# Optimization experiments

Measured on AMD Instinct MI355X. Metric: run time of the kernel, lower is better.

## Reference

```python
import jax, jax.numpy as jnp
import numpy as np

B, D, H = 64, 2048, 2048


def setup_inputs() -> dict:
    key = jax.random.key(0)
    ks = jax.random.split(key, 10)
    s = 1.0 / np.sqrt(D)  # Linear init scale
    # small z scale keeps exp() gates in a sane range
    return {
        "t": jnp.zeros((), jnp.float32),
        "z": jax.random.normal(ks[0], (B, D), jnp.float32) * 0.02,
        "K": jax.random.normal(ks[1], (B, D), jnp.float32) * 0.02,
        "V": jax.random.normal(ks[2], (B, D, D), jnp.float32) * 0.02,
        "Wq": jax.random.normal(ks[3], (D, D), jnp.float32) * s,
        "bq": jnp.zeros((D,), jnp.float32),
        "Wk": jax.random.normal(ks[4], (D, D), jnp.float32) * s,
        "bk": jnp.zeros((D,), jnp.float32),
        "Wv": jax.random.normal(ks[5], (D, D), jnp.float32) * s,
        "bv": jnp.zeros((D,), jnp.float32),
        "W1": jax.random.normal(ks[6], (D, H), jnp.float32) * s,
        "b1": jnp.zeros((H,), jnp.float32),
        "W2": jax.random.normal(ks[7], (H, D), jnp.float32) * (1.0 / np.sqrt(H)),
        "b2": jnp.zeros((D,), jnp.float32),
    }


def reference(t, z, K, V, Wq, bq, Wk, bk, Wv, bv, W1, b1, W2, b2):
    # get_ode_gradient_nn: 2-layer tanh MLP (stand-in for user ode_func_net)
    dz = jnp.tanh(z @ W1 + b1) @ W2 + b2                 # [B, D]
    dK = jnp.exp(z @ Wk + bk)                            # exp gate, [B, D]
    v = z @ Wv + bv                                      # [B, D]
    dV = jnp.einsum("bd,be->bde", v, dK)                # rank-1 outer update, [B, D, D]
    q = jnp.exp(z @ Wq + bq)                             # [B, D]
    a = jnp.sum(q * dK, axis=-1, keepdims=True)          # q . dK, [B, 1]
    dq = q * (dz @ Wq + bq)                              # [B, D]
    da = a + jnp.sum(dq * K, axis=-1, keepdims=True)     # [B, 1]
    dc = jnp.einsum("bde,be->bd", dV, q) + jnp.einsum("bde,be->bd", V, dq)  # [B, D]
    return (dz, da, dc, dK, dV)
```

## Files before the change

### kernel.cpp

```cpp
#include <hip/hip_runtime.h>
#include <cstddef>
#include <math.h>

#define BB 64
#define DD 2048
#define HH 2048
#define BD (BB*DD)
#define WN (2048*2048)

typedef unsigned short u16;
typedef __attribute__((ext_vector_type(8))) short bf16x8;
typedef __attribute__((ext_vector_type(4))) float f32x4;
typedef __attribute__((ext_vector_type(4))) float f4;

__device__ __forceinline__ u16 f2b(float x) {
    union { float f; unsigned u; } v; v.f = x;
    unsigned r = v.u + 0x7FFFu + ((v.u >> 16) & 1u);
    return (u16)(r >> 16);
}

__device__ __forceinline__ void gload16(const void* g, void* l) {
    __builtin_amdgcn_global_load_lds(
        (__attribute__((address_space(1))) void*)g,
        (__attribute__((address_space(3))) void*)l, 16, 0, 0);
}


__global__ __launch_bounds__(256) void wconv(
    const float* __restrict__ W0, const float* __restrict__ W1,
    const float* __restrict__ W2, const float* __restrict__ W3,
    const float* __restrict__ W4, u16* __restrict__ wt)
{
    const float* W;
    switch (blockIdx.z) {
        case 0: W = W0; break; case 1: W = W1; break;
        case 2: W = W2; break; case 3: W = W3; break;
        default: W = W4; break;
    }
    u16* T = wt + (size_t)blockIdx.z * WN;

    __shared__ u16 tile[64][66];
    int k0 = blockIdx.x * 64, n0 = blockIdx.y * 64;
    int t = threadIdx.x;
    {
        int r = t >> 2, c0 = (t & 3) * 16;
        const float* src = W + (size_t)(k0 + r) * DD + n0 + c0;
#pragma unroll
        for (int q = 0; q < 4; ++q) {
            float4 f = *(const float4*)(src + q * 4);
            tile[r][c0 + q*4 + 0] = f2b(f.x);
            tile[r][c0 + q*4 + 1] = f2b(f.y);
            tile[r][c0 + q*4 + 2] = f2b(f.z);
            tile[r][c0 + q*4 + 3] = f2b(f.w);
        }
    }
    __syncthreads();
    {
        int rn = t >> 2, ck = (t & 3) * 16;
        u16 o[16];
#pragma unroll
        for (int j = 0; j < 16; ++j) o[j] = tile[ck + j][rn];
        u16* dst = T + (size_t)(n0 + rn) * DD + k0 + ck;
        *(bf16x8*)dst       = *(bf16x8*)&o[0];
        *(bf16x8*)(dst + 8) = *(bf16x8*)&o[8];
    }
}

__global__ __launch_bounds__(256) void zconv(
    const float* __restrict__ z, u16* __restrict__ zb)
{
    int i = (blockIdx.x * 256 + threadIdx.x) * 4;
    float4 f = *(const float4*)&z[i];
    union { u16 u[4]; uint2 v; } o;
    o.u[0] = f2b(f.x); o.u[1] = f2b(f.y); o.u[2] = f2b(f.z); o.u[3] = f2b(f.w);
    *(uint2*)&zb[i] = o.v;
}

__device__ __forceinline__ void gemm_bf16_body(
    const u16* __restrict__ A, const u16* __restrict__ Wt,
    float* __restrict__ P, int kc)
{
    __shared__ u16 Als[64 * 32];
    __shared__ u16 Wls[64 * 32];
    const int t = threadIdx.x, w = t >> 6, lane = t & 63;
    const int n0 = blockIdx.x * 64;
    const int k0 = blockIdx.y * kc;

    f32x4 acc[4];
#pragma unroll
    for (int mt = 0; mt < 4; ++mt) acc[mt] = (f32x4){0.f, 0.f, 0.f, 0.f};

    const int srow = lane >> 2;
    const int sk   = (lane & 3) * 8;
    const u16* gA = A  + (size_t)(w * 16 + srow) * DD + k0 + sk;
    const u16* gW = Wt + (size_t)(n0 + w * 16 + srow) * DD + k0 + sk;
    u16* lA = &Als[w * 512];
    u16* lW = &Wls[w * 512];

    const int lane15 = lane & 15;
    const int k8 = (lane >> 4) * 8;

    for (int kk = 0; kk < kc; kk += 32) {
        gload16(gA, lA);
        gload16(gW, lW);
        gA += 32; gW += 32;
        __syncthreads();

        bf16x8 bfrag = *(const bf16x8*)&Wls[(w * 16 + lane15) * 32 + k8];
#pragma unroll
        for (int mt = 0; mt < 4; ++mt) {
            bf16x8 afrag = *(const bf16x8*)&Als[(mt * 16 + lane15) * 32 + k8];
            acc[mt] = __builtin_amdgcn_mfma_f32_16x16x32_bf16(
                afrag, bfrag, acc[mt], 0, 0, 0);
        }
        __syncthreads();
    }

    const int col = n0 + w * 16 + lane15;
    const int r4 = (lane >> 4) * 4;
#pragma unroll
    for (int mt = 0; mt < 4; ++mt)
#pragma unroll
        for (int j = 0; j < 4; ++j)
            P[(size_t)(mt * 16 + r4 + j) * DD + col] = acc[mt][j];
}

__global__ __launch_bounds__(256) void gemm_bf16_single(
    const u16* __restrict__ A, const u16* __restrict__ Wt,
    float* __restrict__ part, int kc)
{
    float* P = part + (size_t)blockIdx.y * 64 * DD;
    gemm_bf16_body(A, Wt, P, kc);
}

__global__ __launch_bounds__(256) void gemm_bf16_kv(
    const u16* __restrict__ A, const u16* __restrict__ Wkt,
    const u16* __restrict__ Wvt, float* __restrict__ p0,
    float* __restrict__ p1, int kc)
{
    const u16* Wt = blockIdx.z ? Wvt : Wkt;
    float* P = (blockIdx.z ? p1 : p0) + (size_t)blockIdx.y * 64 * DD;
    gemm_bf16_body(A, Wt, P, kc);
}

__global__ __launch_bounds__(256) void gemm_bf16_q(
    const u16* __restrict__ zb, const u16* __restrict__ dzb,
    const u16* __restrict__ Wqt, float* __restrict__ part, int kc)
{
    const u16* A = blockIdx.z ? dzb : zb;
    float* P = part + ((size_t)blockIdx.y * 128 + blockIdx.z * 64) * DD;
    gemm_bf16_body(A, Wqt, P, kc);
}

__global__ __launch_bounds__(256) void ep_h(
    const float* __restrict__ p, const float* __restrict__ b1,
    u16* __restrict__ hb, int KS)
{
    int i = blockIdx.x * 256 + threadIdx.x;
    float s = b1[i & (DD - 1)];
    for (int ks = 0; ks < KS; ++ks) s += p[(size_t)ks * BD + i];
    hb[i] = f2b(tanhf(s));
}

__global__ __launch_bounds__(256) void ep_dz(
    const float* __restrict__ p, const float* __restrict__ b2,
    float* __restrict__ dz, u16* __restrict__ dzb, int KS)
{
    int i = blockIdx.x * 256 + threadIdx.x;
    float s = b2[i & (DD - 1)];
    for (int ks = 0; ks < KS; ++ks) s += p[(size_t)ks * BD + i];
    dz[i]  = s;
    dzb[i] = f2b(s);
}

__global__ __launch_bounds__(256) void ep_kv(
    const float* __restrict__ pk, const float* __restrict__ pv,
    const float* __restrict__ bk, const float* __restrict__ bv,
    float* __restrict__ dKo, float* __restrict__ vo, int KS)
{
    int i = blockIdx.x * 256 + threadIdx.x;
    int d = i & (DD - 1);
    float sk = 0.f, sv = 0.f;
    for (int ks = 0; ks < KS; ++ks) {
        sk += pk[(size_t)ks * BD + i];
        sv += pv[(size_t)ks * BD + i];
    }
    dKo[i] = expf(sk + bk[d]);
    vo[i]  = sv + bv[d];
}

__global__ __launch_bounds__(256) void ep_q_dq(
    const float* __restrict__ pq, const float* __restrict__ bq,
    float* __restrict__ qo, float* __restrict__ dqo, int KS)
{
    int i = blockIdx.x * 256 + threadIdx.x;
    int b = i >> 11, d = i & (DD - 1);
    float sq = 0.f, sd = 0.f;
    for (int ks = 0; ks < KS; ++ks) {
        const float* P = pq + (size_t)ks * (128 * DD);
        sq += P[(size_t)b * DD + d];
        sd += P[(size_t)(b + 64) * DD + d];
    }
    float bb = bq[d];
    float qv = expf(sq + bb);
    qo[i]  = qv;
    dqo[i] = qv * (sd + bb);
}

template<int MT>
__device__ __forceinline__ void gemm_body_f32(
    const float* __restrict__ A0, const float* __restrict__ A1,
    const float* __restrict__ W, float* __restrict__ part, int kc)
{
    constexpr int KC = 32;
    constexpr int RT = MT / 16;
    __shared__ float As[KC][MT];
    __shared__ float Ws[KC][64];

    const int t  = threadIdx.x;
    const int n0 = blockIdx.x * 64;
    const int k0 = blockIdx.y * kc;
    const int i  = t >> 4;
    const int j  = t & 15;

    float acc[RT][4];
#pragma unroll
    for (int r = 0; r < RT; ++r)
#pragma unroll
        for (int c = 0; c < 4; ++c) acc[r][c] = 0.f;

    for (int kk0 = 0; kk0 < kc; kk0 += KC) {
        {
            int kk = t >> 3;
            int nn = (t & 7) << 3;
            const float* s = W + (size_t)(k0 + kk0 + kk) * DD + n0 + nn;
            *(float4*)&Ws[kk][nn]     = *(const float4*)s;
            *(float4*)&Ws[kk][nn + 4] = *(const float4*)(s + 4);
        }
        if constexpr (MT == 64) {
            int m  = t & 63;
            int kb = (t >> 6) << 3;
            const float* s = A0 + (size_t)m * DD + k0 + kk0 + kb;
            float4 a0 = *(const float4*)s;
            float4 a1 = *(const float4*)(s + 4);
            As[kb+0][m] = a0.x; As[kb+1][m] = a0.y;
            As[kb+2][m] = a0.z; As[kb+3][m] = a0.w;
            As[kb+4][m] = a1.x; As[kb+5][m] = a1.y;
            As[kb+6][m] = a1.z; As[kb+7][m] = a1.w;
        } else {
            int m  = t & 127;
            int kb = (t >> 7) << 4;
            const float* base = (m < 64) ? (A0 + (size_t)m * DD)
                                         : (A1 + (size_t)(m - 64) * DD);
            const float* s = base + k0 + kk0 + kb;
#pragma unroll
            for (int p = 0; p < 4; ++p) {
                float4 av = *(const float4*)(s + p * 4);
                As[kb+p*4+0][m] = av.x; As[kb+p*4+1][m] = av.y;
                As[kb+p*4+2][m] = av.z; As[kb+p*4+3][m] = av.w;
            }
        }
        __syncthreads();
#pragma unroll
        for (int kk = 0; kk < KC; ++kk) {
            float4 wv = *(float4*)&Ws[kk][j << 2];
#pragma unroll
            for (int rq = 0; rq < RT / 4; ++rq) {
                float4 av = *(float4*)&As[kk][i * RT + rq * 4];
                acc[rq*4+0][0] = fmaf(av.x, wv.x, acc[rq*4+0][0]);
                acc[rq*4+0][1] = fmaf(av.x, wv.y, acc[rq*4+0][1]);
                acc[rq*4+0][2] = fmaf(av.x, wv.z, acc[rq*4+0][2]);
                acc[rq*4+0][3] = fmaf(av.x, wv.w, acc[rq*4+0][3]);
                acc[rq*4+1][0] = fmaf(av.y, wv.x, acc[rq*4+1][0]);
                acc[rq*4+1][1] = fmaf(av.y, wv.y, acc[rq*4+1][1]);
                acc[rq*4+1][2] = fmaf(av.y, wv.z, acc[rq*4+1][2]);
                acc[rq*4+1][3] = fmaf(av.y, wv.w, acc[rq*4+1][3]);
                acc[rq*4+2][0] = fmaf(av.z, wv.x, acc[rq*4+2][0]);
                acc[rq*4+2][1] = fmaf(av.z, wv.y, acc[rq*4+2][1]);
                acc[rq*4+2][2] = fmaf(av.z, wv.z, acc[rq*4+2][2]);
                acc[rq*4+2][3] = fmaf(av.z, wv.w, acc[rq*4+2][3]);
                acc[rq*4+3][0] = fmaf(av.w, wv.x, acc[rq*4+3][0]);
                acc[rq*4+3][1] = fmaf(av.w, wv.y, acc[rq*4+3][1]);
                acc[rq*4+3][2] = fmaf(av.w, wv.z, acc[rq*4+3][2]);
                acc[rq*4+3][3] = fmaf(av.w, wv.w, acc[rq*4+3][3]);
            }
        }
        __syncthreads();
    }

    float* P = part + (size_t)blockIdx.y * MT * DD + n0 + (j << 2);
#pragma unroll
    for (int r = 0; r < RT; ++r)
        *(float4*)&P[(size_t)(i * RT + r) * DD] =
            make_float4(acc[r][0], acc[r][1], acc[r][2], acc[r][3]);
}

__global__ __launch_bounds__(256) void gemm64(
    const float* __restrict__ A, const float* __restrict__ W,
    float* __restrict__ part, int kc)
{ gemm_body_f32<64>(A, A, W, part, kc); }

__global__ __launch_bounds__(256) void gemm64_z2(
    const float* __restrict__ A,
    const float* __restrict__ W0, const float* __restrict__ W1,
    float* __restrict__ p0, float* __restrict__ p1, int kc)
{
    const float* W = blockIdx.z ? W1 : W0;
    float*       P = blockIdx.z ? p1 : p0;
    gemm_body_f32<64>(A, A, W, P, kc);
}

__global__ __launch_bounds__(256) void gemm128(
    const float* __restrict__ A0, const float* __restrict__ A1,
    const float* __restrict__ W, float* __restrict__ part, int kc)
{ gemm_body_f32<128>(A0, A1, W, part, kc); }

__global__ __launch_bounds__(256) void epilogue_f32(
    const float* __restrict__ part, const float* __restrict__ bias,
    float* __restrict__ out, int act, int KS)
{
    int i = blockIdx.x * 256 + threadIdx.x;
    float s = bias[i & (DD - 1)];
    for (int ks = 0; ks < KS; ++ks) s += part[(size_t)ks * BD + i];
    if (act == 1) s = tanhf(s);
    out[i] = s;
}

__global__ __launch_bounds__(256) void reduce_a_da(
    const float* __restrict__ q, const float* __restrict__ dK,
    const float* __restrict__ dq, const float* __restrict__ Kin,
    float* __restrict__ a_ws, float* __restrict__ da_out)
{
    int b = blockIdx.x;
    int t = threadIdx.x;
    const float* qb  = q   + (size_t)b * DD;
    const float* dKb = dK  + (size_t)b * DD;
    const float* dqb = dq  + (size_t)b * DD;
    const float* Kb  = Kin + (size_t)b * DD;

    float s1 = 0.f, s2 = 0.f;
    for (int i = t; i < DD; i += 256) {
        s1 = fmaf(qb[i],  dKb[i], s1);
        s2 = fmaf(dqb[i], Kb[i],  s2);
    }
#pragma unroll
    for (int off = 32; off; off >>= 1) {
        s1 += __shfl_down(s1, off);
        s2 += __shfl_down(s2, off);
    }
    __shared__ float r1[4], r2[4];
    if ((t & 63) == 0) { r1[t >> 6] = s1; r2[t >> 6] = s2; }
    __syncthreads();
    if (t == 0) {
        float a  = r1[0] + r1[1] + r1[2] + r1[3];
        float k2 = r2[0] + r2[1] + r2[2] + r2[3];
        a_ws[b]   = a;
        da_out[b] = a + k2;
    }
}

__global__ __launch_bounds__(256) void fused_dv_dc(
    const float* __restrict__ V, const float* __restrict__ v,
    const float* __restrict__ dK, const float* __restrict__ dq,
    const float* __restrict__ a, float* __restrict__ dV,
    float* __restrict__ dc)
{
    int b     = blockIdx.x >> 5;
    int chunk = blockIdx.x & 31;
    int wave  = threadIdx.x >> 6;
    int lane  = threadIdx.x & 63;

    const f4* dK4 = (const f4*)(dK + ((size_t)b << 11));
    const f4* dq4 = (const f4*)(dq + ((size_t)b << 11));
    f4 dKr[8], dqr[8];
#pragma unroll
    for (int u = 0; u < 8; ++u) {
        dKr[u] = dK4[u * 64 + lane];
        dqr[u] = dq4[u * 64 + lane];
    }
    float ab = a[b];
    int row0 = chunk * 64 + wave * 16;

    for (int g = 0; g < 4; ++g) {
        float dot[4];
#pragma unroll
        for (int r2 = 0; r2 < 4; ++r2) {
            int row = row0 + g * 4 + r2;
            size_t off = ((size_t)((b << 11) | row)) << 11;
            const f4* V4  = (const f4*)(V  + off);
            f4*       dV4 = (f4*)(dV + off);
            float vr = v[((size_t)b << 11) + row];
            float d  = 0.f;
#pragma unroll
            for (int u = 0; u < 8; ++u) {
                f4 Vv = __builtin_nontemporal_load(&V4[u * 64 + lane]);
                d += Vv[0] * dqr[u][0] + Vv[1] * dqr[u][1]
                   + Vv[2] * dqr[u][2] + Vv[3] * dqr[u][3];
                f4 o = vr * dKr[u];
                __builtin_nontemporal_store(o, &dV4[u * 64 + lane]);
            }
            dot[r2] = d;
        }
#pragma unroll
        for (int r2 = 0; r2 < 4; ++r2) {
            float d = dot[r2];
#pragma unroll
            for (int s = 32; s; s >>= 1) d += __shfl_down(d, s);
            if (lane == 0) {
                int row = row0 + g * 4 + r2;
                dc[((size_t)b << 11) + row] =
                    v[((size_t)b << 11) + row] * ab + d;
            }
        }
    }
}

extern "C" void kernel_launch(void* const* d_in, const int* in_sizes, int n_in,
                              void* d_out, int out_size, void* d_ws, size_t ws_size,
                              hipStream_t stream)
{
    const float* z   = (const float*)d_in[1];
    const float* Kin = (const float*)d_in[2];
    const float* Vin = (const float*)d_in[3];
    const float* Wq  = (const float*)d_in[4];
    const float* bq  = (const float*)d_in[5];
    const float* Wk  = (const float*)d_in[6];
    const float* bk  = (const float*)d_in[7];
    const float* Wv  = (const float*)d_in[8];
    const float* bv  = (const float*)d_in[9];
    const float* W1  = (const float*)d_in[10];
    const float* b1  = (const float*)d_in[11];
    const float* W2  = (const float*)d_in[12];
    const float* b2  = (const float*)d_in[13];

    float* out   = (float*)d_out;
    float* o_dz  = out;
    float* o_da  = out + BD;
    float* o_dc  = out + BD + BB;
    float* o_dK  = out + 2 * BD + BB;
    float* o_dV  = out + 3 * BD + BB;

    float* ws    = (float*)d_ws;
    float* ws_v  = ws;
    float* ws_q  = ws + BD;
    float* ws_dq = ws + 2 * BD;
    float* ws_a  = ws + 3 * BD;
    float* ws_h  = ws + 3 * BD + 64;
    u16*   zb    = (u16*)(ws + 4 * BD + 64);
    u16*   hb    = zb + BD;
    u16*   dzb   = hb + BD;
    u16*   wt    = dzb + BD;
    float* poolb = (float*)(wt + 5ull * WN);

    const size_t pre_fl = 4ull * BD + 64 + (3ull * BD + 5ull * WN) / 2;

    int KS = 0;
    for (int ks = 16; ks >= 4; ks >>= 1)
        if ((pre_fl + 2ull * ks * BD) * 4ull <= ws_size) { KS = ks; break; }

    dim3 blk(256);
    dim3 gE(BD / 256);

    if (KS) {
        int kc = DD / KS;
        float* p0 = poolb;
        float* p1 = poolb + (size_t)KS * BD;

        dim3 gW(32, 32, 5);
        dim3 gG(32, KS);
        dim3 gG2(32, KS, 2);

        wconv<<<gW, blk, 0, stream>>>(W1, W2, Wk, Wv, Wq, wt);
        zconv<<<dim3(BD / 1024), blk, 0, stream>>>(z, zb);

        u16* W1t = wt;
        u16* W2t = wt + 1ull * WN;
        u16* Wkt = wt + 2ull * WN;
        u16* Wvt = wt + 3ull * WN;
        u16* Wqt = wt + 4ull * WN;

        gemm_bf16_single<<<gG, blk, 0, stream>>>(zb, W1t, p0, kc);
        ep_h<<<gE, blk, 0, stream>>>(p0, b1, hb, KS);

        gemm_bf16_single<<<gG, blk, 0, stream>>>(hb, W2t, p0, kc);
        ep_dz<<<gE, blk, 0, stream>>>(p0, b2, o_dz, dzb, KS);

        gemm_bf16_kv<<<gG2, blk, 0, stream>>>(zb, Wkt, Wvt, p0, p1, kc);
        ep_kv<<<gE, blk, 0, stream>>>(p0, p1, bk, bv, o_dK, ws_v, KS);

        gemm_bf16_q<<<gG2, blk, 0, stream>>>(zb, dzb, Wqt, p0, kc);
        ep_q_dq<<<gE, blk, 0, stream>>>(p0, bq, ws_q, ws_dq, KS);
    } else {
        float* pool = ws + 4 * BD + 64;
        int KSf = 16;
        while (KSf > 1 &&
               ((size_t)(4 * BD + 64) + 2ull * KSf * BD) * 4ull > ws_size)
            KSf >>= 1;
        int kc = DD / KSf;
        float* p0 = pool;
        float* p1 = pool + (size_t)KSf * BD;

        dim3 gG(DD / 64, KSf);
        dim3 gG2(DD / 64, KSf, 2);

        gemm64<<<gG, blk, 0, stream>>>(z, W1, p0, kc);
        epilogue_f32<<<gE, blk, 0, stream>>>(p0, b1, ws_h, 1, KSf);

        gemm64<<<gG, blk, 0, stream>>>(ws_h, W2, p0, kc);
        epilogue_f32<<<gE, blk, 0, stream>>>(p0, b2, o_dz, 0, KSf);

        gemm64_z2<<<gG2, blk, 0, stream>>>(z, Wk, Wv, p0, p1, kc);
        ep_kv<<<gE, blk, 0, stream>>>(p0, p1, bk, bv, o_dK, ws_v, KSf);

        gemm128<<<gG, blk, 0, stream>>>(z, o_dz, Wq, p0, kc);
        ep_q_dq<<<gE, blk, 0, stream>>>(p0, bq, ws_q, ws_dq, KSf);
    }

    reduce_a_da<<<dim3(BB), blk, 0, stream>>>(ws_q, o_dK, ws_dq, Kin, ws_a, o_da);

    fused_dv_dc<<<dim3(BB * 32), blk, 0, stream>>>(Vin, ws_v, o_dK, ws_dq, ws_a,
                                                   o_dV, o_dc);
}
```

Measured before the change: 493.9 us.

## Split fused dV/dc kernel and merge z conversion into weight conversion

The fused kernel that both wrote dV and read V for dc is split into two kernels. dv_write is launched right after the K/V epilogue, and dc_dot runs at the end. The zconv launch is folded into wconv as an extra z-slice of the grid, saving one launch. The split aims to avoid mixing the write and read streams in one kernel, but it adds a separate launch and keeps the same total traffic (256MB write plus 256MB read) on a serial stream, so no overlap is gained.

Measured after the change: 445.7 us. -9.8%, faster.

```diff
diff --git a/kernel.cpp b/kernel.cpp
--- a/kernel.cpp
+++ b/kernel.cpp
@@ -29,8 +29,24 @@
 __global__ __launch_bounds__(256) void wconv(
     const float* __restrict__ W0, const float* __restrict__ W1,
     const float* __restrict__ W2, const float* __restrict__ W3,
-    const float* __restrict__ W4, u16* __restrict__ wt)
-{
+    const float* __restrict__ W4, u16* __restrict__ wt,
+    const float* __restrict__ z, u16* __restrict__ zb)
+{
+    int t = threadIdx.x;
+    if (blockIdx.z == 5) {
+        if (blockIdx.y != 0 || blockIdx.x >= 32) return;
+        int i0 = blockIdx.x * 4096 + t * 16;
+        u16 o[16];
+#pragma unroll
+        for (int q = 0; q < 4; ++q) {
+            float4 f = *(const float4*)&z[i0 + q * 4];
+            o[q*4+0] = f2b(f.x); o[q*4+1] = f2b(f.y);
+            o[q*4+2] = f2b(f.z); o[q*4+3] = f2b(f.w);
+        }
+        *(bf16x8*)&zb[i0]     = *(bf16x8*)&o[0];
+        *(bf16x8*)&zb[i0 + 8] = *(bf16x8*)&o[8];
+        return;
+    }
     const float* W;
     switch (blockIdx.z) {
         case 0: W = W0; break; case 1: W = W1; break;
@@ -41,7 +57,6 @@
 
     __shared__ u16 tile[64][66];
     int k0 = blockIdx.x * 64, n0 = blockIdx.y * 64;
-    int t = threadIdx.x;
     {
         int r = t >> 2, c0 = (t & 3) * 16;
         const float* src = W + (size_t)(k0 + r) * DD + n0 + c0;
@@ -64,16 +79,6 @@
         *(bf16x8*)dst       = *(bf16x8*)&o[0];
         *(bf16x8*)(dst + 8) = *(bf16x8*)&o[8];
     }
-}
-
-__global__ __launch_bounds__(256) void zconv(
-    const float* __restrict__ z, u16* __restrict__ zb)
-{
-    int i = (blockIdx.x * 256 + threadIdx.x) * 4;
-    float4 f = *(const float4*)&z[i];
-    union { u16 u[4]; uint2 v; } o;
-    o.u[0] = f2b(f.x); o.u[1] = f2b(f.y); o.u[2] = f2b(f.z); o.u[3] = f2b(f.w);
-    *(uint2*)&zb[i] = o.v;
 }
 
 __device__ __forceinline__ void gemm_bf16_body(
@@ -359,11 +364,9 @@
     }
 }
 
-__global__ __launch_bounds__(256) void fused_dv_dc(
-    const float* __restrict__ V, const float* __restrict__ v,
-    const float* __restrict__ dK, const float* __restrict__ dq,
-    const float* __restrict__ a, float* __restrict__ dV,
-    float* __restrict__ dc)
+__global__ __launch_bounds__(256) void dv_write(
+    const float* __restrict__ v, const float* __restrict__ dK,
+    float* __restrict__ dV)
 {
     int b     = blockIdx.x >> 5;
     int chunk = blockIdx.x & 31;
@@ -371,33 +374,52 @@
     int lane  = threadIdx.x & 63;
 
     const f4* dK4 = (const f4*)(dK + ((size_t)b << 11));
+    f4 dKr[8];
+#pragma unroll
+    for (int u = 0; u < 8; ++u) dKr[u] = dK4[u * 64 + lane];
+
+    int row0 = chunk * 64 + wave * 16;
+    for (int rr = 0; rr < 16; ++rr) {
+        int row = row0 + rr;
+        float vr = v[((size_t)b << 11) + row];
+        f4* dV4 = (f4*)(dV + (((size_t)((b << 11) | row)) << 11));
+#pragma unroll
+        for (int u = 0; u < 8; ++u) {
+            f4 o = vr * dKr[u];
+            __builtin_nontemporal_store(o, &dV4[u * 64 + lane]);
+        }
+    }
+}
+
+__global__ __launch_bounds__(256) void dc_dot(
+    const float* __restrict__ V, const float* __restrict__ v,
+    const float* __restrict__ dq, const float* __restrict__ a,
+    float* __restrict__ dc)
+{
+    int b     = blockIdx.x >> 5;
+    int chunk = blockIdx.x & 31;
+    int wave  = threadIdx.x >> 6;
+    int lane  = threadIdx.x & 63;
+
     const f4* dq4 = (const f4*)(dq + ((size_t)b << 11));
-    f4 dKr[8], dqr[8];
-#pragma unroll
-    for (int u = 0; u < 8; ++u) {
-        dKr[u] = dK4[u * 64 + lane];
-        dqr[u] = dq4[u * 64 + lane];
-    }
+    f4 dqr[8];
+#pragma unroll
+    for (int u = 0; u < 8; ++u) dqr[u] = dq4[u * 64 + lane];
     float ab = a[b];
+
     int row0 = chunk * 64 + wave * 16;
-
     for (int g = 0; g < 4; ++g) {
         float dot[4];
 #pragma unroll
         for (int r2 = 0; r2 < 4; ++r2) {
             int row = row0 + g * 4 + r2;
-            size_t off = ((size_t)((b << 11) | row)) << 11;
-            const f4* V4  = (const f4*)(V  + off);
-            f4*       dV4 = (f4*)(dV + off);
-            float vr = v[((size_t)b << 11) + row];
-            float d  = 0.f;
+            const f4* V4 = (const f4*)(V + (((size_t)((b << 11) | row)) << 11));
+            float d = 0.f;
 #pragma unroll
             for (int u = 0; u < 8; ++u) {
                 f4 Vv = __builtin_nontemporal_load(&V4[u * 64 + lane]);
                 d += Vv[0] * dqr[u][0] + Vv[1] * dqr[u][1]
                    + Vv[2] * dqr[u][2] + Vv[3] * dqr[u][3];
-                f4 o = vr * dKr[u];
-                __builtin_nontemporal_store(o, &dV4[u * 64 + lane]);
             }
             dot[r2] = d;
         }
@@ -466,12 +488,11 @@
         float* p0 = poolb;
         float* p1 = poolb + (size_t)KS * BD;
 
-        dim3 gW(32, 32, 5);
+        dim3 gW(32, 32, 6);
         dim3 gG(32, KS);
         dim3 gG2(32, KS, 2);
 
-        wconv<<<gW, blk, 0, stream>>>(W1, W2, Wk, Wv, Wq, wt);
-        zconv<<<dim3(BD / 1024), blk, 0, stream>>>(z, zb);
+        wconv<<<gW, blk, 0, stream>>>(W1, W2, Wk, Wv, Wq, wt, z, zb);
 
         u16* W1t = wt;
         u16* W2t = wt + 1ull * WN;
@@ -487,6 +508,8 @@
 
         gemm_bf16_kv<<<gG2, blk, 0, stream>>>(zb, Wkt, Wvt, p0, p1, kc);
         ep_kv<<<gE, blk, 0, stream>>>(p0, p1, bk, bv, o_dK, ws_v, KS);
+
+        dv_write<<<dim3(BB * 32), blk, 0, stream>>>(ws_v, o_dK, o_dV);
 
         gemm_bf16_q<<<gG2, blk, 0, stream>>>(zb, dzb, Wqt, p0, kc);
         ep_q_dq<<<gE, blk, 0, stream>>>(p0, bq, ws_q, ws_dq, KS);
@@ -512,12 +535,13 @@
         gemm64_z2<<<gG2, blk, 0, stream>>>(z, Wk, Wv, p0, p1, kc);
         ep_kv<<<gE, blk, 0, stream>>>(p0, p1, bk, bv, o_dK, ws_v, KSf);
 
+        dv_write<<<dim3(BB * 32), blk, 0, stream>>>(ws_v, o_dK, o_dV);
+
         gemm128<<<gG, blk, 0, stream>>>(z, o_dz, Wq, p0, kc);
         ep_q_dq<<<gE, blk, 0, stream>>>(p0, bq, ws_q, ws_dq, KSf);
     }
 
     reduce_a_da<<<dim3(BB), blk, 0, stream>>>(ws_q, o_dK, ws_dq, Kin, ws_a, o_da);
 
-    fused_dv_dc<<<dim3(BB * 32), blk, 0, stream>>>(Vin, ws_v, o_dK, ws_dq, ws_a,
-                                                   o_dV, o_dc);
-}
+    dc_dot<<<dim3(BB * 32), blk, 0, stream>>>(Vin, ws_v, ws_dq, ws_a, o_dc);
+}
```
